# Kernel optimization log

Measured on AMD Instinct MI355X. Metric: run time of the kernel, lower is better.

Reference implementation:

```python
import jax, jax.numpy as jnp
import numpy as np

N_FEAT = 64      # number of continuous features
N_BINS = 255     # bin edges per feature (EBM default) -> 256 score slots incl. OOV
N_PAIRS = 32     # interaction terms
BATCH = 262144


def _bin_indices(edges, x):
    """TF Discretization (searchsorted right) + IntegerLookup(vocab=range(B), OOV->0).
    edges: [N, B] sorted per row; x: [batch, N] -> int32 [batch, N] in [0, B]."""
    idx = jax.vmap(lambda e, col: jnp.searchsorted(e, col, side='right'),
                   in_axes=(0, 1), out_axes=1)(edges, x)  # [batch, N], values 0..B
    B = edges.shape[1]
    # IntegerLookup: value v in {0..B-1} -> v+1 ; value B (not in vocab) -> OOV index 0
    return jnp.where(idx < B, idx + 1, 0)


def setup_inputs() -> dict:
    key = jax.random.key(0)
    ks = jax.random.split(key, 6)
    x = jax.random.normal(ks[0], (BATCH, N_FEAT), dtype=jnp.float32)
    edges = jnp.sort(jax.random.normal(ks[1], (N_FEAT, N_BINS), dtype=jnp.float32), axis=1)
    pair_edges = jnp.sort(jax.random.normal(ks[2], (N_FEAT, N_BINS), dtype=jnp.float32), axis=1)
    w = jax.random.normal(ks[3], (N_FEAT, N_BINS + 1), dtype=jnp.float32) * 0.1
    tables = jax.random.normal(ks[4], (N_PAIRS, N_BINS + 1, N_BINS + 1), dtype=jnp.float32) * 0.1
    pairs = jax.random.randint(ks[5], (N_PAIRS, 2), 0, N_FEAT, dtype=jnp.int32)
    bias = jnp.zeros((1,), dtype=jnp.float32)
    return {"x": x, "edges": edges, "w": w, "pair_edges": pair_edges,
            "pairs": pairs, "tables": tables, "bias": bias}


def reference(x, edges, w, pair_edges, pairs, tables, bias):
    # --- per-feature main effects: one_hot(idx) @ Dense(1) == gather w[f, idx] ---
    idx = _bin_indices(edges, x)                                  # [batch, N]
    feat = w[jnp.arange(N_FEAT)[None, :], idx]                    # [batch, N]
    # --- pairwise interactions: gather_nd on [L, R] lookup tables ---
    pidx = _bin_indices(pair_edges, x)                            # [batch, N]
    li = pidx[:, pairs[:, 0]]                                     # [batch, P]
    ri = pidx[:, pairs[:, 1]]                                     # [batch, P]
    inter = tables[jnp.arange(N_PAIRS)[None, :], li, ri]          # [batch, P]
    # --- BiasLayer: reduce_sum(concat, axis=1) + bias, then sigmoid ---
    logits = jnp.sum(feat, axis=1) + jnp.sum(inter, axis=1) + bias[0]
    return jax.nn.sigmoid(logits)                                  # [batch]
```

## Files before the change

### kernel.cpp

```cpp
#include <hip/hip_runtime.h>
#include <hip/hip_fp16.h>

#define NBINS 255
#define NPAIRS 32
#define BIGF 3.0e38f


__global__ void ebm_prep(const float* __restrict__ edges,
                         const float* __restrict__ pair_edges,
                         const float* __restrict__ w,
                         float* __restrict__ ws) {
    int tid = blockIdx.x * blockDim.x + threadIdx.x;
    int f = tid >> 8, j = tid & 255;
    float* E  = ws;
    float* PE = ws + 16384;
    float* ME = ws + 32768;
    float* MP = ws + 36864;
    float* CU = ws + 40960;
    float* CP = ws + 41984;
    __half* W = (__half*)(ws + 43008);
    E[tid]  = (j < NBINS) ? edges[f * NBINS + j]      : BIGF;
    PE[tid] = (j < NBINS) ? pair_edges[f * NBINS + j] : BIGF;
    int src = (j < 255) ? j + 1 : 0;
    W[tid]  = __float2half(w[f * 256 + src]);
    if (j < 64) {
        int idx = 4 * j + 3;
        ME[f * 64 + j] = (idx < NBINS) ? edges[f * NBINS + idx]      : BIGF;
        MP[f * 64 + j] = (idx < NBINS) ? pair_edges[f * NBINS + idx] : BIGF;
    }
    if (j < 16) {
        CU[f * 16 + j] = (j < 15) ? edges[f * NBINS + 16 * j + 15]      : BIGF;
        CP[f * 16 + j] = (j < 15) ? pair_edges[f * NBINS + 16 * j + 15] : BIGF;
    }
}

__global__ void ebm_prep_tables(const float* __restrict__ tables,
                                unsigned short* __restrict__ o) {
    int i = blockIdx.x * blockDim.x + threadIdx.x;
    int b = i & 255, a = (i >> 8) & 255, p = i >> 16;
    int ra = (a < 255) ? a + 1 : 0;
    int rb = (b < 255) ? b + 1 : 0;
    o[i] = __half_as_ushort(__float2half(tables[(p << 16) + (ra << 8) + rb]));
}

__device__ __forceinline__ unsigned pick16(const unsigned* pw, int s) {
    unsigned v01 = (s & 1) ? pw[1]  : pw[0];
    unsigned v23 = (s & 1) ? pw[3]  : pw[2];
    unsigned v45 = (s & 1) ? pw[5]  : pw[4];
    unsigned v67 = (s & 1) ? pw[7]  : pw[6];
    unsigned v89 = (s & 1) ? pw[9]  : pw[8];
    unsigned vab = (s & 1) ? pw[11] : pw[10];
    unsigned vcd = (s & 1) ? pw[13] : pw[12];
    unsigned vef = (s & 1) ? pw[15] : pw[14];
    unsigned w0 = (s & 2) ? v23 : v01;
    unsigned w1 = (s & 2) ? v67 : v45;
    unsigned w2 = (s & 2) ? vab : v89;
    unsigned w3 = (s & 2) ? vef : vcd;
    unsigned u0 = (s & 4) ? w1 : w0;
    unsigned u1 = (s & 4) ? w3 : w2;
    return (s & 8) ? u1 : u0;
}

__global__ __launch_bounds__(1024) void ebm_main(
    const float* __restrict__ x,
    const int*   __restrict__ pairs,
    const float* __restrict__ tables_f32,
    const float* __restrict__ bias,
    const float* __restrict__ ws,
    const __half* __restrict__ T16,
    int useT16,
    float*       __restrict__ out) {

    __shared__ float  sE[16384];
    __shared__ float  sPE[16384];
    __shared__ float4 sME[1024];
    __shared__ float4 sMP[1024];

    int tid = threadIdx.x;
    {
        const float4* w4 = (const float4*)ws;
        float4* dE = (float4*)sE;
        float4* dP = (float4*)sPE;
        for (int i = tid; i < 4096; i += 1024) {
            dE[i] = w4[i];
            dP[i] = w4[4096 + i];
        }
        if (tid < 1024) {
            sME[tid] = w4[8192 + tid];
            sMP[tid] = w4[9216 + tid];
        }
    }
    const float*  CU = ws + 40960;
    const float*  CP = ws + 41984;
    const __half* Wg = (const __half*)(ws + 43008);
    float bias0 = bias[0];

    __syncthreads();

    int row = blockIdx.x * 1024 + tid;
    const float4* x4 = (const float4*)x + row * 16;
    const float4* sE4 = (const float4*)sE;
    const float4* sP4 = (const float4*)sPE;

    float acc = 0.f;
    unsigned pw[16];

    float4 xg = x4[0];
#pragma unroll
    for (int g = 0; g < 16; ++g) {
        float4 xnext = xg;
        if (g < 15) xnext = x4[g + 1];
        float xf[4] = {xg.x, xg.y, xg.z, xg.w};

        int t[4];
#pragma unroll
        for (int j = 0; j < 4; ++j) {
            const float* cu = CU + (4 * g + j) * 16;
            int tt = 0;
#pragma unroll
            for (int k = 0; k < 15; ++k) tt += (xf[j] >= cu[k]);
            t[j] = tt;
        }
        int t2[4];
#pragma unroll
        for (int j = 0; j < 4; ++j) {
            const float* cp = CP + (4 * g + j) * 16;
            int tt = 0;
#pragma unroll
            for (int k = 0; k < 15; ++k) tt += (xf[j] >= cp[k]);
            t2[j] = tt;
        }
        float4 mu[4], mp[4];
#pragma unroll
        for (int j = 0; j < 4; ++j) mu[j] = sME[(4 * g + j) * 16 + t[j]];
#pragma unroll
        for (int j = 0; j < 4; ++j) mp[j] = sMP[(4 * g + j) * 16 + t2[j]];
        int lo[4], lo2[4];
        float4 fu[4], fp[4];
#pragma unroll
        for (int j = 0; j < 4; ++j) {
            int m = (xf[j] >= mu[j].x) + (xf[j] >= mu[j].y) + (xf[j] >= mu[j].z);
            lo[j] = 4 * t[j] + m;
            fu[j] = sE4[(4 * g + j) * 64 + lo[j]];
        }
#pragma unroll
        for (int j = 0; j < 4; ++j) {
            int m = (xf[j] >= mp[j].x) + (xf[j] >= mp[j].y) + (xf[j] >= mp[j].z);
            lo2[j] = 4 * t2[j] + m;
            fp[j] = sP4[(4 * g + j) * 64 + lo2[j]];
        }
#pragma unroll
        for (int j = 0; j < 4; ++j) {
            int c = 4 * lo[j] + (xf[j] >= fu[j].x) + (xf[j] >= fu[j].y) +
                    (xf[j] >= fu[j].z) + (xf[j] >= fu[j].w);
            acc += __half2float(Wg[(4 * g + j) * 256 + c]);
        }
        unsigned pword = 0;
#pragma unroll
        for (int j = 0; j < 4; ++j) {
            int c2 = 4 * lo2[j] + (xf[j] >= fp[j].x) + (xf[j] >= fp[j].y) +
                     (xf[j] >= fp[j].z) + (xf[j] >= fp[j].w);
            pword |= (unsigned)c2 << (8 * j);
        }
        pw[g] = pword;
        xg = xnext;
    }

    if (useT16) {
#pragma unroll
        for (int p = 0; p < NPAIRS; ++p) {
            int a = pairs[2 * p], b = pairs[2 * p + 1];
            unsigned wa = pick16(pw, a >> 2);
            unsigned wb = pick16(pw, b >> 2);
            int li = (wa >> ((a & 3) * 8)) & 255;
            int ri = (wb >> ((b & 3) * 8)) & 255;
            acc += __half2float(T16[(p << 16) + (li << 8) + ri]);
        }
    } else {
#pragma unroll
        for (int p = 0; p < NPAIRS; ++p) {
            int a = pairs[2 * p], b = pairs[2 * p + 1];
            unsigned wa = pick16(pw, a >> 2);
            unsigned wb = pick16(pw, b >> 2);
            int li = (wa >> ((a & 3) * 8)) & 255;
            int ri = (wb >> ((b & 3) * 8)) & 255;
            int lb = (li < 255) ? li + 1 : 0;
            int rb = (ri < 255) ? ri + 1 : 0;
            acc += tables_f32[(p << 16) + (lb << 8) + rb];
        }
    }

    out[row] = 1.0f / (1.0f + __expf(-(acc + bias0)));
}

extern "C" void kernel_launch(void* const* d_in, const int* in_sizes, int n_in,
                              void* d_out, int out_size, void* d_ws, size_t ws_size,
                              hipStream_t stream) {
    const float* x          = (const float*)d_in[0];
    const float* edges      = (const float*)d_in[1];
    const float* w          = (const float*)d_in[2];
    const float* pair_edges = (const float*)d_in[3];
    const int*   pairs      = (const int*)d_in[4];
    const float* tables     = (const float*)d_in[5];
    const float* bias       = (const float*)d_in[6];
    float* out = (float*)d_out;
    float* ws  = (float*)d_ws;

    int useT16 = (ws_size >= (size_t)4399104) ? 1 : 0;
    __half* T16 = (__half*)((char*)d_ws + 204800);

    ebm_prep<<<64, 256, 0, stream>>>(edges, pair_edges, w, ws);
    if (useT16) {
        ebm_prep_tables<<<2048, 1024, 0, stream>>>(tables, (unsigned short*)T16);
    }
    ebm_main<<<256, 1024, 0, stream>>>(x, pairs, tables, bias, ws, T16, useT16, out);
}
```

Baseline: 193.5 us.

## Replace three-level bin search with two-level strided smem layout; vectorize table prep

The main kernel now stores each feature's edges in shared memory in a transposed layout where the four float4 values for a coarse bucket are 16 float4s apart. A thread can then load the 16 candidate edges after the coarse 15-comparison search with four independent smem reads, replacing the dependent middle level and its sME/sMP arrays. Features are processed in pairs to interleave work. The table-conversion prep kernel handles 8 elements per thread with a 16-byte vector store and launches fewer blocks. The cost is more comparisons and smem reads per feature, possible bank conflicts from the strided layout, and higher register pressure.

New measurement: 209.5 us. 1.08x slower.

```diff
diff --git a/kernel.cpp b/kernel.cpp
--- a/kernel.cpp
+++ b/kernel.cpp
@@ -36,11 +36,27 @@
 
 __global__ void ebm_prep_tables(const float* __restrict__ tables,
                                 unsigned short* __restrict__ o) {
-    int i = blockIdx.x * blockDim.x + threadIdx.x;
-    int b = i & 255, a = (i >> 8) & 255, p = i >> 16;
+    int i2 = blockIdx.x * blockDim.x + threadIdx.x;
+    int p = i2 >> 13, a = (i2 >> 5) & 255, b0 = (i2 & 31) << 3;
     int ra = (a < 255) ? a + 1 : 0;
-    int rb = (b < 255) ? b + 1 : 0;
-    o[i] = __half_as_ushort(__float2half(tables[(p << 16) + (ra << 8) + rb]));
+    const float* src = tables + (p << 16) + (ra << 8);
+    float f[8];
+#pragma unroll
+    for (int k = 0; k < 8; ++k) {
+        int b = b0 + k;
+        int rb = (b < 255) ? b + 1 : 0;
+        f[k] = src[rb];
+    }
+    uint4 v;
+    v.x = (unsigned)__half_as_ushort(__float2half(f[1])) << 16 |
+          (unsigned)__half_as_ushort(__float2half(f[0]));
+    v.y = (unsigned)__half_as_ushort(__float2half(f[3])) << 16 |
+          (unsigned)__half_as_ushort(__float2half(f[2]));
+    v.z = (unsigned)__half_as_ushort(__float2half(f[5])) << 16 |
+          (unsigned)__half_as_ushort(__float2half(f[4]));
+    v.w = (unsigned)__half_as_ushort(__float2half(f[7])) << 16 |
+          (unsigned)__half_as_ushort(__float2half(f[6]));
+    *(uint4*)(o + ((size_t)i2 << 3)) = v;
 }
 
 __device__ __forceinline__ unsigned pick16(const unsigned* pw, int s) {
@@ -71,10 +87,8 @@
     int useT16,
     float*       __restrict__ out) {
 
-    __shared__ float  sE[16384];
-    __shared__ float  sPE[16384];
-    __shared__ float4 sME[1024];
-    __shared__ float4 sMP[1024];
+    __shared__ float sE[16384];
+    __shared__ float sPE[16384];
 
     int tid = threadIdx.x;
     {
@@ -82,12 +96,10 @@
         float4* dE = (float4*)sE;
         float4* dP = (float4*)sPE;
         for (int i = tid; i < 4096; i += 1024) {
-            dE[i] = w4[i];
-            dP[i] = w4[4096 + i];
-        }
-        if (tid < 1024) {
-            sME[tid] = w4[8192 + tid];
-            sMP[tid] = w4[9216 + tid];
+            int f = i >> 6, j = i & 63;
+            int d = (f << 6) + ((j & 3) << 4) + (j >> 2);
+            dE[d] = w4[i];
+            dP[d] = w4[4096 + i];
         }
     }
     const float*  CU = ws + 40960;
@@ -98,7 +110,7 @@
     __syncthreads();
 
     int row = blockIdx.x * 1024 + tid;
-    const float4* x4 = (const float4*)x + row * 16;
+    const float4* x4  = (const float4*)x + row * 16;
     const float4* sE4 = (const float4*)sE;
     const float4* sP4 = (const float4*)sPE;
 
@@ -111,56 +123,55 @@
         float4 xnext = xg;
         if (g < 15) xnext = x4[g + 1];
         float xf[4] = {xg.x, xg.y, xg.z, xg.w};
-
-        int t[4];
-#pragma unroll
-        for (int j = 0; j < 4; ++j) {
-            const float* cu = CU + (4 * g + j) * 16;
-            int tt = 0;
-#pragma unroll
-            for (int k = 0; k < 15; ++k) tt += (xf[j] >= cu[k]);
-            t[j] = tt;
-        }
-        int t2[4];
-#pragma unroll
-        for (int j = 0; j < 4; ++j) {
-            const float* cp = CP + (4 * g + j) * 16;
-            int tt = 0;
-#pragma unroll
-            for (int k = 0; k < 15; ++k) tt += (xf[j] >= cp[k]);
-            t2[j] = tt;
-        }
-        float4 mu[4], mp[4];
-#pragma unroll
-        for (int j = 0; j < 4; ++j) mu[j] = sME[(4 * g + j) * 16 + t[j]];
-#pragma unroll
-        for (int j = 0; j < 4; ++j) mp[j] = sMP[(4 * g + j) * 16 + t2[j]];
-        int lo[4], lo2[4];
-        float4 fu[4], fp[4];
-#pragma unroll
-        for (int j = 0; j < 4; ++j) {
-            int m = (xf[j] >= mu[j].x) + (xf[j] >= mu[j].y) + (xf[j] >= mu[j].z);
-            lo[j] = 4 * t[j] + m;
-            fu[j] = sE4[(4 * g + j) * 64 + lo[j]];
-        }
-#pragma unroll
-        for (int j = 0; j < 4; ++j) {
-            int m = (xf[j] >= mp[j].x) + (xf[j] >= mp[j].y) + (xf[j] >= mp[j].z);
-            lo2[j] = 4 * t2[j] + m;
-            fp[j] = sP4[(4 * g + j) * 64 + lo2[j]];
-        }
-#pragma unroll
-        for (int j = 0; j < 4; ++j) {
-            int c = 4 * lo[j] + (xf[j] >= fu[j].x) + (xf[j] >= fu[j].y) +
-                    (xf[j] >= fu[j].z) + (xf[j] >= fu[j].w);
-            acc += __half2float(Wg[(4 * g + j) * 256 + c]);
-        }
         unsigned pword = 0;
-#pragma unroll
-        for (int j = 0; j < 4; ++j) {
-            int c2 = 4 * lo2[j] + (xf[j] >= fp[j].x) + (xf[j] >= fp[j].y) +
-                     (xf[j] >= fp[j].z) + (xf[j] >= fp[j].w);
-            pword |= (unsigned)c2 << (8 * j);
+
+#pragma unroll
+        for (int s = 0; s < 2; ++s) {
+            float x0 = xf[2 * s], x1 = xf[2 * s + 1];
+            int f0 = 4 * g + 2 * s, f1 = f0 + 1;
+
+            int t0 = 0, t1 = 0;
+            const float* cu0 = CU + f0 * 16;
+            const float* cu1 = CU + f1 * 16;
+#pragma unroll
+            for (int k = 0; k < 15; ++k) {
+                t0 += (x0 >= cu0[k]);
+                t1 += (x1 >= cu1[k]);
+            }
+            float4 a0[4], a1[4];
+#pragma unroll
+            for (int k = 0; k < 4; ++k) a0[k] = sE4[(f0 << 6) + (k << 4) + t0];
+#pragma unroll
+            for (int k = 0; k < 4; ++k) a1[k] = sE4[(f1 << 6) + (k << 4) + t1];
+            int u0 = 0, u1 = 0;
+            const float* cp0 = CP + f0 * 16;
+            const float* cp1 = CP + f1 * 16;
+#pragma unroll
+            for (int k = 0; k < 15; ++k) {
+                u0 += (x0 >= cp0[k]);
+                u1 += (x1 >= cp1[k]);
+            }
+            int c0 = t0 << 4, c1 = t1 << 4;
+#pragma unroll
+            for (int k = 0; k < 4; ++k) {
+                c0 += (x0 >= a0[k].x) + (x0 >= a0[k].y) + (x0 >= a0[k].z) + (x0 >= a0[k].w);
+                c1 += (x1 >= a1[k].x) + (x1 >= a1[k].y) + (x1 >= a1[k].z) + (x1 >= a1[k].w);
+            }
+            acc += __half2float(Wg[f0 * 256 + c0]);
+            acc += __half2float(Wg[f1 * 256 + c1]);
+            float4 b0[4], b1[4];
+#pragma unroll
+            for (int k = 0; k < 4; ++k) b0[k] = sP4[(f0 << 6) + (k << 4) + u0];
+#pragma unroll
+            for (int k = 0; k < 4; ++k) b1[k] = sP4[(f1 << 6) + (k << 4) + u1];
+            int d0 = u0 << 4, d1 = u1 << 4;
+#pragma unroll
+            for (int k = 0; k < 4; ++k) {
+                d0 += (x0 >= b0[k].x) + (x0 >= b0[k].y) + (x0 >= b0[k].z) + (x0 >= b0[k].w);
+                d1 += (x1 >= b1[k].x) + (x1 >= b1[k].y) + (x1 >= b1[k].z) + (x1 >= b1[k].w);
+            }
+            pword |= (unsigned)d0 << (8 * (2 * s));
+            pword |= (unsigned)d1 << (8 * (2 * s + 1));
         }
         pw[g] = pword;
         xg = xnext;
@@ -211,7 +222,7 @@
 
     ebm_prep<<<64, 256, 0, stream>>>(edges, pair_edges, w, ws);
     if (useT16) {
-        ebm_prep_tables<<<2048, 1024, 0, stream>>>(tables, (unsigned short*)T16);
+        ebm_prep_tables<<<256, 1024, 0, stream>>>(tables, (unsigned short*)T16);
     }
     ebm_main<<<256, 1024, 0, stream>>>(x, pairs, tables, bias, ws, T16, useT16, out);
 }
```
